# Kernel tuning notes

Measured on AMD Instinct MI355X. Metric: run time of the kernel, lower is better.

## Reference

```python
import jax, jax.numpy as jnp
import numpy as np

T, B, V = 50, 128, 8000          # seq_len, batch, inputDimSize
A = 728                          # numAncestors
NEMB = V + A                     # rows of W_emb
E, H, ATT, C, L = 128, 128, 100, 283, 5


def setup_inputs() -> dict:
    key = jax.random.key(0)
    ks = jax.random.split(key, 12)
    x = jax.random.normal(ks[0], (T, B, V), jnp.float32)
    mask = jnp.ones((T, B), jnp.float32)
    leaves = jax.random.randint(ks[1], (V, L), 0, NEMB)
    ancestors = jax.random.randint(ks[2], (V, L), 0, NEMB)
    W_emb = jax.random.uniform(ks[3], (NEMB, E), jnp.float32)
    W_attention = jax.random.uniform(ks[4], (2 * E, ATT), jnp.float32)
    b_attention = jnp.zeros((ATT,), jnp.float32)
    v_attention = jax.random.uniform(ks[5], (ATT,), jnp.float32)
    gru_w_ih = jax.random.normal(ks[6], (3 * H, E), jnp.float32) * 0.1
    gru_w_hh = jax.random.normal(ks[7], (3 * H, H), jnp.float32) * 0.1
    gru_b_ih = jnp.zeros((3 * H,), jnp.float32)
    gru_b_hh = jnp.zeros((3 * H,), jnp.float32)
    W_output = jax.random.uniform(ks[8], (H, C), jnp.float32) * 0.1
    b_output = jnp.zeros((C,), jnp.float32)
    return {"x": x, "mask": mask, "W_emb": W_emb,
            "W_attention": W_attention, "b_attention": b_attention,
            "v_attention": v_attention, "gru_w_ih": gru_w_ih,
            "gru_w_hh": gru_w_hh, "gru_b_ih": gru_b_ih,
            "gru_b_hh": gru_b_hh, "W_output": W_output,
            "b_output": b_output, "leaves": leaves, "ancestors": ancestors}


def reference(x, mask, W_emb, W_attention, b_attention, v_attention,
              gru_w_ih, gru_w_hh, gru_b_ih, gru_b_hh,
              W_output, b_output, leaves, ancestors):
    # --- Attention over ontology ancestors (gather + MLP + softmax + reduce) ---
    le = W_emb[leaves]       # [V, L, E]
    an = W_emb[ancestors]    # [V, L, E]
    att_in = jnp.concatenate([le, an], axis=-1)              # [V, L, 2E]
    mlp = jnp.tanh(att_in @ W_attention + b_attention)       # [V, L, ATT]
    pre = mlp @ v_attention                                  # [V, L]
    att = jax.nn.softmax(pre, axis=1)                        # softmax over ancestors
    emb = jnp.einsum('vle,vl->ve', an, att)                  # [V, E]

    # --- project multi-hot visits into embedding space ---
    x_emb = jnp.tanh(jnp.einsum('tbv,ve->tbe', x, emb))      # [T, B, E]

    # --- torch-style single-layer GRU via scan (time-major) ---
    def cell(h, xt):
        gx = xt @ gru_w_ih.T + gru_b_ih                      # [B, 3H]
        gh = h @ gru_w_hh.T + gru_b_hh
        xr, xz, xn = jnp.split(gx, 3, axis=-1)
        hr, hz, hn = jnp.split(gh, 3, axis=-1)
        r = jax.nn.sigmoid(xr + hr)
        z = jax.nn.sigmoid(xz + hz)
        n = jnp.tanh(xn + r * hn)
        h_new = (1.0 - z) * n + z * h
        return h_new, h_new

    h0 = jnp.zeros((B, H), x_emb.dtype)
    _, hidden = jax.lax.scan(cell, h0, x_emb)                # [T, B, H]

    # dropout_rate = 0 -> identity
    # exp / sum == softmax over the class dim
    out = jax.nn.softmax(hidden @ W_output + b_output, axis=2)  # [T, B, C]
    return out * mask[:, :, None]
```

## Files before the change

### kernel.cpp

```cpp
#include <hip/hip_runtime.h>


typedef unsigned short u16;
typedef unsigned int   u32;
typedef short bf16x8 __attribute__((ext_vector_type(8)));
typedef float f32x4  __attribute__((ext_vector_type(4)));

typedef __attribute__((address_space(1))) u32 gas_u32;
typedef __attribute__((address_space(3))) u32 las_u32;

union U4 { u32 u[4]; bf16x8 v; uint4 q; };

__device__ __forceinline__ float uaf(u32 u){ union{u32 u; float f;} c; c.u=u; return c.f; }
__device__ __forceinline__ u32 fau(float f){ union{u32 u; float f;} c; c.f=f; return c.u; }
__device__ __forceinline__ u16 f2bf(float f){ u32 u=fau(f); return (u16)((u + 0x7fffu + ((u>>16)&1u))>>16); }
__device__ __forceinline__ float sigm(float x){ return 1.f/(1.f+__expf(-x)); }

__device__ __forceinline__ void gll16(const void* g, void* l){
    __builtin_amdgcn_global_load_lds((const gas_u32*)g, (las_u32*)l, 16, 0, 0);
}

__device__ __forceinline__ void split8(const float* f, bf16x8* hi, bf16x8* lo){
    U4 H, L;
    #pragma unroll
    for (int j=0;j<4;++j){
        float f0=f[2*j], f1=f[2*j+1];
        u32 u0=fau(f0), u1=fau(f1);
        u32 t0=u0+0x7fffu+((u0>>16)&1u);
        u32 t1=u1+0x7fffu+((u1>>16)&1u);
        u32 h1=t1&0xffff0000u;
        H.u[j]=(t0>>16)|h1;
        float l0=f0-uaf(t0&0xffff0000u);
        float l1=f1-uaf(h1);
        u32 v0=fau(l0), v1=fau(l1);
        u32 s0=v0+0x7fffu+((v0>>16)&1u);
        u32 s1=v1+0x7fffu+((v1>>16)&1u);
        L.u[j]=(s0>>16)|(s1&0xffff0000u);
    }
    *hi=H.v; *lo=L.v;
}

__device__ __forceinline__ void split1(float f, u16& h, u16& l){
    u32 u=fau(f); u32 t=u+0x7fffu+((u>>16)&1u); h=(u16)(t>>16);
    float lf=f-uaf(t&0xffff0000u); l=f2bf(lf);
}

#define MFMA(a,b,c) __builtin_amdgcn_mfma_f32_16x16x32_bf16(a,b,c,0,0,0)

__global__ __launch_bounds__(256,1) void prep_watt_kernel(
    const float* __restrict__ W_att, u16* __restrict__ WT_h, u16* __restrict__ WT_l)
{
    int n=blockIdx.x, k=threadIdx.x;
    float f = (n<100)? W_att[k*100+n] : 0.f;
    u16 h,l; split1(f,h,l);
    WT_h[n*256+k]=h; WT_l[n*256+k]=l;
}

__global__ __launch_bounds__(256,1) void prep_whh_kernel(
    const float* __restrict__ whh, u32* __restrict__ out)
{
    int i=blockIdx.x*256+threadIdx.x;
    int j=i>>6, p=i&63;
    u32 a=(u32)f2bf(whh[j*128+2*p]);
    u32 b=(u32)f2bf(whh[j*128+2*p+1]);
    out[i]=a|(b<<16);
}

__global__ __launch_bounds__(256,1) void transpose_wih_kernel(
    const float* __restrict__ w_ih, float* __restrict__ w_ihT)
{
    int i=blockIdx.x*256+threadIdx.x;
    int e=i/384, j=i-e*384;
    w_ihT[i]=w_ih[j*128+e];
}

__global__ __launch_bounds__(256,1) void attn_mlp_kernel(
    const float* __restrict__ W_emb, const float* __restrict__ b_att,
    const float* __restrict__ v_att, const int* __restrict__ leaves,
    const int* __restrict__ anc, const u16* __restrict__ WT_h,
    const u16* __restrict__ WT_l, float* __restrict__ emb_f)
{
    __shared__ __align__(16) char smem[61440];
    short* Ah=(short*)smem;
    short* Al=(short*)(smem+16384);
    short* Bh=(short*)(smem+32768);
    short* Bl=(short*)(smem+47104);
    float* mlp_s=(float*)smem;
    __shared__ float s_pre[128];
    __shared__ float s_vatt[112];
    __shared__ float s_attw[128];
    __shared__ int   s_leaf[128], s_anc[128];

    const int tid=threadIdx.x;
    const int wave=tid>>6, lane=tid&63;
    const int vb5=blockIdx.x*125;

    if (tid<125){ s_leaf[tid]=leaves[vb5+tid]; s_anc[tid]=anc[vb5+tid]; }
    else if (tid<128){ s_leaf[tid]=leaves[vb5]; s_anc[tid]=anc[vb5]; }
    if (tid<100) s_vatt[tid]=v_att[tid];

    f32x4 acc[2][7];
    const f32x4 zf={0.f,0.f,0.f,0.f};
    #pragma unroll
    for (int mi=0;mi<2;++mi)
        #pragma unroll
        for (int ni=0;ni<7;++ni) acc[mi][ni]=zf;

    const int fr=lane&15, fq=lane>>4;

    for (int kc=0;kc<4;++kc){
        __syncthreads();
        {
            int r=tid>>1, seg=tid&1;
            int src=(kc<2)? s_leaf[r] : s_anc[r];
            const float* srcp = W_emb + (size_t)src*128 + (kc&1)*64 + seg*32;
            float buf[32];
            #pragma unroll
            for (int i=0;i<8;++i) *(f32x4*)(buf+4*i) = *(const f32x4*)(srcp+4*i);
            #pragma unroll
            for (int j=0;j<4;++j){
                bf16x8 hv, lv; split8(buf+8*j, &hv, &lv);
                U4 H,L; H.v=hv; L.v=lv;
                *(uint4*)&Ah[r*64+seg*32+j*8] = H.q;
                *(uint4*)&Al[r*64+seg*32+j*8] = L.q;
            }
        }
        for (int c=wave;c<14;c+=4){
            size_t go=(size_t)(c*8+(lane>>3))*512 + (size_t)kc*128 + (size_t)(lane&7)*16;
            gll16((const char*)WT_h+go, Bh+c*512);
            gll16((const char*)WT_l+go, Bl+c*512);
        }
        __syncthreads();

        #pragma unroll
        for (int ks=0;ks<2;++ks){
            bf16x8 ah[2],al[2],bh[7],bl[7];
            #pragma unroll
            for (int mi=0;mi<2;++mi){
                int row=wave*32+mi*16+fr;
                ah[mi]=*(const bf16x8*)&Ah[row*64+ks*32+fq*8];
                al[mi]=*(const bf16x8*)&Al[row*64+ks*32+fq*8];
            }
            #pragma unroll
            for (int ni=0;ni<7;++ni){
                int rowb=ni*16+fr;
                bh[ni]=*(const bf16x8*)&Bh[rowb*64+ks*32+fq*8];
                bl[ni]=*(const bf16x8*)&Bl[rowb*64+ks*32+fq*8];
            }
            #pragma unroll
            for (int mi=0;mi<2;++mi)
                #pragma unroll
                for (int ni=0;ni<7;++ni){
                    acc[mi][ni]=MFMA(ah[mi],bh[ni],acc[mi][ni]);
                    acc[mi][ni]=MFMA(ah[mi],bl[ni],acc[mi][ni]);
                    acc[mi][ni]=MFMA(al[mi],bh[ni],acc[mi][ni]);
                }
        }
    }
    __syncthreads();
    #pragma unroll
    for (int ni=0;ni<7;++ni){
        int col=ni*16+fr;
        float bb=(col<100)? b_att[col] : 0.f;
        #pragma unroll
        for (int mi=0;mi<2;++mi){
            int rb=wave*32+mi*16+fq*4;
            #pragma unroll
            for (int r=0;r<4;++r)
                mlp_s[(rb+r)*112+col]=tanhf(acc[mi][ni][r]+bb);
        }
    }
    __syncthreads();
    if (tid<128){
        float s=0.f;
        for (int n=0;n<100;++n) s+=mlp_s[tid*112+n]*s_vatt[n];
        s_pre[tid]=s;
    }
    __syncthreads();
    if (tid<25){
        float p[5], mx=-1e30f;
        #pragma unroll
        for (int l=0;l<5;++l){ p[l]=s_pre[tid*5+l]; mx=fmaxf(mx,p[l]); }
        float s=0.f;
        #pragma unroll
        for (int l=0;l<5;++l){ p[l]=__expf(p[l]-mx); s+=p[l]; }
        float inv=1.f/s;
        #pragma unroll
        for (int l=0;l<5;++l) s_attw[tid*5+l]=p[l]*inv;
    }
    __syncthreads();
    for (int o=tid;o<3200;o+=256){
        int v=o>>7, e=o&127;
        float s=0.f;
        #pragma unroll
        for (int l=0;l<5;++l)
            s += s_attw[v*5+l]*W_emb[(size_t)s_anc[v*5+l]*128+e];
        emb_f[(size_t)(blockIdx.x*25+v)*128+e]=s;
    }
}

__global__ __launch_bounds__(256,1) void emb_split_kernel(
    const float* __restrict__ emb_f, u16* __restrict__ hiT, u16* __restrict__ loT)
{
    __shared__ float tile[64*128];
    const int tid=threadIdx.x;
    const int vb=blockIdx.x*64;
    for (int i=tid;i<2048;i+=256){
        int row=i>>5, q=i&31;
        *(f32x4*)&tile[row*128+q*4] = *(const f32x4*)&emb_f[(size_t)(vb+row)*128+q*4];
    }
    __syncthreads();
    u32* hw=(u32*)hiT; u32* lw=(u32*)loT;
    for (int o=tid;o<4096;o+=256){
        int e=o>>5, p=o&31;
        float f0=tile[(2*p)*128+e], f1=tile[(2*p+1)*128+e];
        u16 h0,l0,h1,l1; split1(f0,h0,l0); split1(f1,h1,l1);
        size_t base=(size_t)e*4000 + (size_t)(vb>>1) + p;
        hw[base]=(u32)h0|((u32)h1<<16);
        lw[base]=(u32)l0|((u32)l1<<16);
    }
}

__global__ __launch_bounds__(256,4) void gemm_xemb_kernel(
    const float* __restrict__ x, const u16* __restrict__ bhT, const u16* __restrict__ blT,
    float* __restrict__ partials)
{
    __shared__ __align__(16) float Asf[32*64];
    __shared__ __align__(16) short Bh[128*64];
    __shared__ __align__(16) short Bl[128*64];

    const int tid=threadIdx.x, wave=tid>>6, lane=tid&63;
    const int mt=blockIdx.x%200, ks=blockIdx.x/200;
    const int mbase=mt*32;
    const int k0=ks*1600;

    f32x4 acc[2][2];
    const f32x4 zf={0.f,0.f,0.f,0.f};
    #pragma unroll
    for (int i=0;i<2;++i)
        #pragma unroll
        for (int j=0;j<2;++j) acc[i][j]=zf;

    const char* xb=(const char*)x;
    const char* bhb=(const char*)bhT;
    const char* blb=(const char*)blT;
    const int fr=lane&15, fq=lane>>4;
    const int nbase=wave*32;

    for (int kk=k0; kk<k0+1600; kk+=64){
        __syncthreads();
        #pragma unroll
        for (int ii=0;ii<2;++ii){
            int L=(wave*2+ii)*64+lane;
            int r=L>>4, c=(L&15)^(r&15);
            gll16(xb + ((size_t)(mbase+r)*8000 + kk + c*4)*4, (char*)Asf + (size_t)L*16);
        }
        #pragma unroll
        for (int ii=0;ii<4;++ii){
            int L=(wave*4+ii)*64+lane;
            int r=L>>3, c=(L&7)^(r&7);
            size_t go=((size_t)r*8000 + kk + c*8)*2;
            gll16(bhb+go, (char*)Bh + (size_t)L*16);
            gll16(blb+go, (char*)Bl + (size_t)L*16);
        }
        __syncthreads();

        #pragma unroll
        for (int kh=0;kh<2;++kh){
            bf16x8 ah[2],al[2],bh[2],bl[2];
            #pragma unroll
            for (int mi=0;mi<2;++mi){
                int row=mi*16+fr;
                int c0=kh*8+fq*2;
                float buf[8];
                *(f32x4*)&buf[0]=*(const f32x4*)&Asf[(row*16+((c0  )^(row&15)))*4];
                *(f32x4*)&buf[4]=*(const f32x4*)&Asf[(row*16+((c0+1)^(row&15)))*4];
                split8(buf,&ah[mi],&al[mi]);
            }
            #pragma unroll
            for (int ni=0;ni<2;++ni){
                int rowb=nbase+ni*16+fr;
                int ch=rowb*8+((kh*4+fq)^(rowb&7));
                bh[ni]=*(const bf16x8*)&Bh[ch*8];
                bl[ni]=*(const bf16x8*)&Bl[ch*8];
            }
            #pragma unroll
            for (int mi=0;mi<2;++mi)
                #pragma unroll
                for (int ni=0;ni<2;++ni){
                    acc[mi][ni]=MFMA(ah[mi],bh[ni],acc[mi][ni]);
                    acc[mi][ni]=MFMA(ah[mi],bl[ni],acc[mi][ni]);
                    acc[mi][ni]=MFMA(al[mi],bh[ni],acc[mi][ni]);
                }
        }
    }

    float* pout=partials + ((size_t)ks*6400+mbase)*128;
    #pragma unroll
    for (int mi=0;mi<2;++mi)
        #pragma unroll
        for (int ni=0;ni<2;++ni)
            #pragma unroll
            for (int r=0;r<4;++r)
                pout[(size_t)(mi*16+fq*4+r)*128 + nbase+ni*16+fr]=acc[mi][ni][r];
}

__global__ __launch_bounds__(256,1) void sum_tanh_kernel(
    const float* __restrict__ partials, float* __restrict__ x_emb)
{
    int i=blockIdx.x*256+threadIdx.x;
    float s=0.f;
    #pragma unroll
    for (int k=0;k<5;++k) s+=partials[(size_t)k*819200+i];
    x_emb[i]=tanhf(s);
}

__global__ __launch_bounds__(128,1) void gx_gemm_kernel(
    const float* __restrict__ x_emb, const float* __restrict__ w_ihT,
    const float* __restrict__ b_ih, float* __restrict__ GX)
{
    __shared__ float sx[2048];
    const int tid=threadIdx.x;
    const int rb=blockIdx.x*16;
    for (int i=tid;i<2048;i+=128) sx[i]=x_emb[(size_t)rb*128+i];
    __syncthreads();

    float acc0[16],acc1[16],acc2[16];
    #pragma unroll
    for (int r=0;r<16;++r){ acc0[r]=0.f; acc1[r]=0.f; acc2[r]=0.f; }
    for (int e=0;e<128;++e){
        float w0=w_ihT[e*384+tid];
        float w1=w_ihT[e*384+tid+128];
        float w2=w_ihT[e*384+tid+256];
        #pragma unroll
        for (int r=0;r<16;++r){
            float xv=sx[r*128+e];
            acc0[r]=fmaf(xv,w0,acc0[r]);
            acc1[r]=fmaf(xv,w1,acc1[r]);
            acc2[r]=fmaf(xv,w2,acc2[r]);
        }
    }
    float b0=b_ih[tid], b1=b_ih[tid+128], b2=b_ih[tid+256];
    #pragma unroll
    for (int r=0;r<16;++r){
        float* gp=GX+(size_t)(rb+r)*384;
        gp[tid]=acc0[r]+b0;
        gp[tid+128]=acc1[r]+b1;
        gp[tid+256]=acc2[r]+b2;
    }
}

__global__ __launch_bounds__(384,1) void gru_scan_kernel(
    const u32* __restrict__ whh_p, const float* __restrict__ b_hh,
    const float* __restrict__ GX, float* __restrict__ hidden)
{
    __shared__ __align__(16) u16 shb[128];
    __shared__ float sgh[384];
    const int tid=threadIdx.x, b=blockIdx.x;

    float wf[128];
    #pragma unroll
    for (int q=0;q<64;++q){
        u32 u=whh_p[tid*64+q];
        wf[2*q]  =uaf(u<<16);
        wf[2*q+1]=uaf(u&0xffff0000u);
    }
    float hreg=0.f;
    if (tid<128) shb[tid]=0;
    const float bb=b_hh[tid];
    __syncthreads();

    for (int t=0;t<50;++t){
        float gx0=0.f,gx1=0.f,gx2=0.f;
        if (tid<128){
            const float* gp=GX+((size_t)t*128+b)*384;
            gx0=gp[tid]; gx1=gp[128+tid]; gx2=gp[256+tid];
        }
        float acc=0.f;
        #pragma unroll
        for (int p=0;p<16;++p){
            U4 c; c.v=*(const bf16x8*)&shb[p*8];
            #pragma unroll
            for (int j=0;j<4;++j){
                u32 u=c.u[j];
                acc=fmaf(uaf(u<<16),         wf[p*8+2*j],   acc);
                acc=fmaf(uaf(u&0xffff0000u), wf[p*8+2*j+1], acc);
            }
        }
        sgh[tid]=acc+bb;
        __syncthreads();
        if (tid<128){
            float r=sigm(gx0+sgh[tid]);
            float z=sigm(gx1+sgh[128+tid]);
            float n=tanhf(gx2+r*sgh[256+tid]);
            float hn=(1.f-z)*n+z*hreg;
            hreg=hn;
            hidden[((size_t)t*128+b)*128+tid]=hn;
            shb[tid]=f2bf(hn);
        }
        __syncthreads();
    }
}

__global__ __launch_bounds__(128,1) void logits_kernel(
    const float* __restrict__ hidden, const float* __restrict__ W_out,
    const float* __restrict__ b_out, float* __restrict__ logits)
{
    __shared__ float shd[2048];
    const int tid=threadIdx.x;
    const int rb=blockIdx.x*16;
    for (int i=tid;i<2048;i+=128) shd[i]=hidden[(size_t)rb*128+i];
    __syncthreads();

    const int c0=tid, c1=tid+128, c2=tid+256;
    const bool v2=(c2<283);
    float acc0[16],acc1[16],acc2[16];
    #pragma unroll
    for (int r=0;r<16;++r){ acc0[r]=0.f; acc1[r]=0.f; acc2[r]=0.f; }
    for (int h=0;h<128;++h){
        const float* wr=W_out+h*283;
        float w0=wr[c0];
        float w1=wr[c1];
        float w2=v2? wr[c2] : 0.f;
        #pragma unroll
        for (int r=0;r<16;++r){
            float hv=shd[r*128+h];
            acc0[r]=fmaf(hv,w0,acc0[r]);
            acc1[r]=fmaf(hv,w1,acc1[r]);
            acc2[r]=fmaf(hv,w2,acc2[r]);
        }
    }
    float b0=b_out[c0], b1=b_out[c1], b2v=v2? b_out[c2] : 0.f;
    #pragma unroll
    for (int r=0;r<16;++r){
        float* lp=logits+(size_t)(rb+r)*283;
        lp[c0]=acc0[r]+b0;
        lp[c1]=acc1[r]+b1;
        if (v2) lp[c2]=acc2[r]+b2v;
    }
}

__global__ __launch_bounds__(256,1) void softmax_mask_kernel(
    const float* __restrict__ logits, const float* __restrict__ mask,
    float* __restrict__ out)
{
    const int wave=threadIdx.x>>6, lane=threadIdx.x&63;
    const int m=blockIdx.x*4+wave;
    const float* lp=logits+(size_t)m*283;
    float v[5];
    float mx=-1e30f;
    #pragma unroll
    for (int i=0;i<5;++i){
        int c=lane+i*64;
        v[i]=(c<283)? lp[c] : -1e30f;
        mx=fmaxf(mx,v[i]);
    }
    #pragma unroll
    for (int off=32;off>0;off>>=1) mx=fmaxf(mx,__shfl_xor(mx,off,64));
    float s=0.f;
    #pragma unroll
    for (int i=0;i<5;++i){
        int c=lane+i*64;
        v[i]=(c<283)? __expf(v[i]-mx) : 0.f;
        s+=v[i];
    }
    #pragma unroll
    for (int off=32;off>0;off>>=1) s+=__shfl_xor(s,off,64);
    const float sc=mask[m]/s;
    float* op=out+(size_t)m*283;
    #pragma unroll
    for (int i=0;i<5;++i){
        int c=lane+i*64;
        if (c<283) op[c]=v[i]*sc;
    }
}

extern "C" void kernel_launch(void* const* d_in, const int* in_sizes, int n_in,
                              void* d_out, int out_size, void* d_ws, size_t ws_size,
                              hipStream_t stream) {
    const float* x      = (const float*)d_in[0];
    const float* mask   = (const float*)d_in[1];
    const float* W_emb  = (const float*)d_in[2];
    const float* W_att  = (const float*)d_in[3];
    const float* b_att  = (const float*)d_in[4];
    const float* v_att  = (const float*)d_in[5];
    const float* w_ih   = (const float*)d_in[6];
    const float* w_hh   = (const float*)d_in[7];
    const float* b_ih   = (const float*)d_in[8];
    const float* b_hh   = (const float*)d_in[9];
    const float* W_out  = (const float*)d_in[10];
    const float* b_out  = (const float*)d_in[11];
    const int* leaves   = (const int*)d_in[12];
    const int* anc      = (const int*)d_in[13];
    float* out = (float*)d_out;

    char* w = (char*)d_ws;
    u16*   WT_h    = (u16*)(w + 0);
    u16*   WT_l    = (u16*)(w + 57344);
    u32*   whh_p   = (u32*)(w + 114688);
    float* w_ihT   = (float*)(w + 212992);
    u16*   emb_hiT = (u16*)(w + 409600);
    u16*   emb_loT = (u16*)(w + 2457600);
    float* x_emb   = (float*)(w + 4505600);
    float* hidden  = (float*)(w + 7782400);
    float* emb_f   = (float*)(w + 11059200);
    float* partials= (float*)(w + 11059200);
    float* GX      = (float*)(w + 11059200);
    float* logits  = (float*)(w + 11059200);

    prep_watt_kernel<<<112, 256, 0, stream>>>(W_att, WT_h, WT_l);
    prep_whh_kernel<<<96, 256, 0, stream>>>(w_hh, whh_p);
    transpose_wih_kernel<<<192, 256, 0, stream>>>(w_ih, w_ihT);
    attn_mlp_kernel<<<320, 256, 0, stream>>>(W_emb, b_att, v_att, leaves, anc,
                                             WT_h, WT_l, emb_f);
    emb_split_kernel<<<125, 256, 0, stream>>>(emb_f, emb_hiT, emb_loT);
    gemm_xemb_kernel<<<1000, 256, 0, stream>>>(x, emb_hiT, emb_loT, partials);
    sum_tanh_kernel<<<3200, 256, 0, stream>>>(partials, x_emb);
    gx_gemm_kernel<<<400, 128, 0, stream>>>(x_emb, w_ihT, b_ih, GX);
    gru_scan_kernel<<<128, 384, 0, stream>>>(whh_p, b_hh, GX, hidden);
    logits_kernel<<<400, 128, 0, stream>>>(hidden, W_out, b_out, logits);
    softmax_mask_kernel<<<1600, 256, 0, stream>>>(logits, mask, out);
}
```

Baseline: 529.3 us.

## Fuse split-K reduction into GX GEMM and softmax into logits kernel

Folds the split-K partial-sum plus tanh step into the input-projection GEMM's shared-memory load, and keeps logits in shared memory so softmax and masking run in the same kernel. This removes two kernel launches and the global round-trips for x_emb and logits. The global_load_lds addressing in the x·emb GEMM is also rewritten to use a per-wave uniform LDS base, and workspace buffers are moved to non-overlapping offsets. The fused kernels run with only 400 blocks, so they expose less parallelism than the separate kernels did.

```diff
diff --git a/kernel.cpp b/kernel.cpp
--- a/kernel.cpp
+++ b/kernel.cpp
@@ -247,21 +247,29 @@
     const int fr=lane&15, fq=lane>>4;
     const int nbase=wave*32;
 
+    const int ar = lane>>4;
+    const int ac0 = lane&15;
+    const int br = lane>>3;
+    const int bc0 = lane&7;
+
     for (int kk=k0; kk<k0+1600; kk+=64){
         __syncthreads();
         #pragma unroll
         for (int ii=0;ii<2;++ii){
-            int L=(wave*2+ii)*64+lane;
-            int r=L>>4, c=(L&15)^(r&15);
-            gll16(xb + ((size_t)(mbase+r)*8000 + kk + c*4)*4, (char*)Asf + (size_t)L*16);
+            int t=wave*2+ii;
+            int r=t*4+ar;
+            int c=ac0^(r&15);
+            gll16(xb + ((size_t)(mbase+r)*8000 + kk + c*4)*4,
+                  (char*)Asf + (size_t)t*1024);
         }
         #pragma unroll
         for (int ii=0;ii<4;++ii){
-            int L=(wave*4+ii)*64+lane;
-            int r=L>>3, c=(L&7)^(r&7);
+            int s=wave*4+ii;
+            int r=s*8+br;
+            int c=bc0^(r&7);
             size_t go=((size_t)r*8000 + kk + c*8)*2;
-            gll16(bhb+go, (char*)Bh + (size_t)L*16);
-            gll16(blb+go, (char*)Bl + (size_t)L*16);
+            gll16(bhb+go, (char*)Bh + (size_t)s*1024);
+            gll16(blb+go, (char*)Bl + (size_t)s*1024);
         }
         __syncthreads();
 
@@ -305,24 +313,20 @@
                 pout[(size_t)(mi*16+fq*4+r)*128 + nbase+ni*16+fr]=acc[mi][ni][r];
 }
 
-__global__ __launch_bounds__(256,1) void sum_tanh_kernel(
-    const float* __restrict__ partials, float* __restrict__ x_emb)
-{
-    int i=blockIdx.x*256+threadIdx.x;
-    float s=0.f;
-    #pragma unroll
-    for (int k=0;k<5;++k) s+=partials[(size_t)k*819200+i];
-    x_emb[i]=tanhf(s);
-}
-
-__global__ __launch_bounds__(128,1) void gx_gemm_kernel(
-    const float* __restrict__ x_emb, const float* __restrict__ w_ihT,
+__global__ __launch_bounds__(128,1) void sumtanh_gx_kernel(
+    const float* __restrict__ partials, const float* __restrict__ w_ihT,
     const float* __restrict__ b_ih, float* __restrict__ GX)
 {
     __shared__ float sx[2048];
     const int tid=threadIdx.x;
     const int rb=blockIdx.x*16;
-    for (int i=tid;i<2048;i+=128) sx[i]=x_emb[(size_t)rb*128+i];
+    for (int i=tid;i<2048;i+=128){
+        size_t o=(size_t)rb*128+i;
+        float s=0.f;
+        #pragma unroll
+        for (int k=0;k<5;++k) s+=partials[(size_t)k*819200+o];
+        sx[i]=tanhf(s);
+    }
     __syncthreads();
 
     float acc0[16],acc1[16],acc2[16];
@@ -402,11 +406,13 @@
     }
 }
 
-__global__ __launch_bounds__(128,1) void logits_kernel(
+__global__ __launch_bounds__(128,1) void logits_softmax_kernel(
     const float* __restrict__ hidden, const float* __restrict__ W_out,
-    const float* __restrict__ b_out, float* __restrict__ logits)
+    const float* __restrict__ b_out, const float* __restrict__ mask,
+    float* __restrict__ out)
 {
     __shared__ float shd[2048];
+    __shared__ float slog[16*288];
     const int tid=threadIdx.x;
     const int rb=blockIdx.x*16;
     for (int i=tid;i<2048;i+=128) shd[i]=hidden[(size_t)rb*128+i];
@@ -433,45 +439,43 @@
     float b0=b_out[c0], b1=b_out[c1], b2v=v2? b_out[c2] : 0.f;
     #pragma unroll
     for (int r=0;r<16;++r){
-        float* lp=logits+(size_t)(rb+r)*283;
-        lp[c0]=acc0[r]+b0;
-        lp[c1]=acc1[r]+b1;
-        if (v2) lp[c2]=acc2[r]+b2v;
-    }
-}
-
-__global__ __launch_bounds__(256,1) void softmax_mask_kernel(
-    const float* __restrict__ logits, const float* __restrict__ mask,
-    float* __restrict__ out)
-{
-    const int wave=threadIdx.x>>6, lane=threadIdx.x&63;
-    const int m=blockIdx.x*4+wave;
-    const float* lp=logits+(size_t)m*283;
-    float v[5];
-    float mx=-1e30f;
-    #pragma unroll
-    for (int i=0;i<5;++i){
-        int c=lane+i*64;
-        v[i]=(c<283)? lp[c] : -1e30f;
-        mx=fmaxf(mx,v[i]);
-    }
-    #pragma unroll
-    for (int off=32;off>0;off>>=1) mx=fmaxf(mx,__shfl_xor(mx,off,64));
-    float s=0.f;
-    #pragma unroll
-    for (int i=0;i<5;++i){
-        int c=lane+i*64;
-        v[i]=(c<283)? __expf(v[i]-mx) : 0.f;
-        s+=v[i];
-    }
-    #pragma unroll
-    for (int off=32;off>0;off>>=1) s+=__shfl_xor(s,off,64);
-    const float sc=mask[m]/s;
-    float* op=out+(size_t)m*283;
-    #pragma unroll
-    for (int i=0;i<5;++i){
-        int c=lane+i*64;
-        if (c<283) op[c]=v[i]*sc;
+        slog[r*288+c0]=acc0[r]+b0;
+        slog[r*288+c1]=acc1[r]+b1;
+        if (v2) slog[r*288+c2]=acc2[r]+b2v;
+    }
+    __syncthreads();
+
+    const int wv=tid>>6, lane=tid&63;
+    #pragma unroll
+    for (int rr=0;rr<8;++rr){
+        int r=wv*8+rr;
+        int m=rb+r;
+        float v[5];
+        float mx=-1e30f;
+        #pragma unroll
+        for (int i=0;i<5;++i){
+            int c=lane+i*64;
+            v[i]=(c<283)? slog[r*288+c] : -1e30f;
+            mx=fmaxf(mx,v[i]);
+        }
+        #pragma unroll
+        for (int off=32;off>0;off>>=1) mx=fmaxf(mx,__shfl_xor(mx,off,64));
+        float s=0.f;
+        #pragma unroll
+        for (int i=0;i<5;++i){
+            int c=lane+i*64;
+            v[i]=(c<283)? __expf(v[i]-mx) : 0.f;
+            s+=v[i];
+        }
+        #pragma unroll
+        for (int off=32;off>0;off>>=1) s+=__shfl_xor(s,off,64);
+        const float sc=mask[m]/s;
+        float* op=out+(size_t)m*283;
+        #pragma unroll
+        for (int i=0;i<5;++i){
+            int c=lane+i*64;
+            if (c<283) op[c]=v[i]*sc;
+        }
     }
 }
 
@@ -501,12 +505,10 @@
     float* w_ihT   = (float*)(w + 212992);
     u16*   emb_hiT = (u16*)(w + 409600);
     u16*   emb_loT = (u16*)(w + 2457600);
-    float* x_emb   = (float*)(w + 4505600);
-    float* hidden  = (float*)(w + 7782400);
-    float* emb_f   = (float*)(w + 11059200);
-    float* partials= (float*)(w + 11059200);
-    float* GX      = (float*)(w + 11059200);
-    float* logits  = (float*)(w + 11059200);
+    float* emb_f   = (float*)(w + 4505600);
+    float* partials= (float*)(w + 8601600);
+    float* GX      = (float*)(w + 24985600);
+    float* hidden  = (float*)(w + 34816000);
 
     prep_watt_kernel<<<112, 256, 0, stream>>>(W_att, WT_h, WT_l);
     prep_whh_kernel<<<96, 256, 0, stream>>>(w_hh, whh_p);
@@ -515,9 +517,7 @@
                                              WT_h, WT_l, emb_f);
     emb_split_kernel<<<125, 256, 0, stream>>>(emb_f, emb_hiT, emb_loT);
     gemm_xemb_kernel<<<1000, 256, 0, stream>>>(x, emb_hiT, emb_loT, partials);
-    sum_tanh_kernel<<<3200, 256, 0, stream>>>(partials, x_emb);
-    gx_gemm_kernel<<<400, 128, 0, stream>>>(x_emb, w_ihT, b_ih, GX);
+    sumtanh_gx_kernel<<<400, 128, 0, stream>>>(partials, w_ihT, b_ih, GX);
     gru_scan_kernel<<<128, 384, 0, stream>>>(whh_p, b_hh, GX, hidden);
-    logits_kernel<<<400, 128, 0, stream>>>(hidden, W_out, b_out, logits);
-    softmax_mask_kernel<<<1600, 256, 0, stream>>>(logits, mask, out);
-}
+    logits_softmax_kernel<<<400, 128, 0, stream>>>(hidden, W_out, b_out, mask, out);
+}
```

Result: no change. 523.7 us (-1.1%).
